# Optimization experiments

Measured on AMD Instinct MI355X. Metric: run time of the kernel, lower is better.

Reference implementation:

```python
import jax, jax.numpy as jnp
import numpy as np

B, T, D_IN, D_RNN, D_HID, D_OUT = 4096, 512, 16, 64, 128, 1

def setup_inputs() -> dict:
    key = jax.random.key(0)
    ks = jax.random.split(key, 8)
    s = 0.05  # RandomNormal init stddev
    return {
        "x":  jax.random.normal(ks[0], (B, T, D_IN), jnp.float32),
        "Wx": jax.random.normal(ks[1], (D_IN, D_RNN), jnp.float32) * s,
        "Wh": jax.random.normal(ks[2], (D_RNN, D_RNN), jnp.float32) * s,
        "b":  jnp.zeros((D_RNN,), jnp.float32),
        "W1": jax.random.normal(ks[3], (3 * D_RNN, D_HID), jnp.float32) * s,
        "b1": jnp.zeros((D_HID,), jnp.float32),
        "W2": jax.random.normal(ks[4], (D_HID, D_OUT), jnp.float32) * s,
        "b2": jnp.zeros((D_OUT,), jnp.float32),
    }

def reference(x, Wx, Wh, b, W1, b1, W2, b2):
    # SimpleRNN: h_t = tanh(x_t @ Wx + h_{t-1} @ Wh + b)
    batch = x.shape[0]
    xw = jnp.einsum('bti,ih->tbh', x, Wx) + b  # precompute input projection, time-major
    h0 = jnp.zeros((batch, Wh.shape[0]), x.dtype)

    def step(h, xw_t):
        h_new = jnp.tanh(xw_t + h @ Wh)
        return h_new, h_new

    _, hs = jax.lax.scan(step, h0, xw)          # hs: [T, B, rnn_dim]
    last3 = jnp.transpose(hs[-3:], (1, 0, 2))   # [B, 3, rnn_dim]
    out = jnp.tanh(last3.reshape(batch, -1))    # flatten + tanh
    # dropout is identity at inference
    out = jnp.tanh(out @ W1 + b1)
    out = out @ W2 + b2
    return out
```

## Files before the change

kernel.cpp:

```cpp
#include <hip/hip_runtime.h>
#include <cstdint>
#include <cstddef>

#define TSEQ 512
#define DRNN 64
#define DIN  16
#define FSTRIDE 66

typedef float    f32x4 __attribute__((ext_vector_type(4)));
typedef unsigned u32x4 __attribute__((ext_vector_type(4)));
typedef _Float16 f16x8 __attribute__((ext_vector_type(8)));

#define MFMA16(A, B, C) __builtin_amdgcn_mfma_f32_16x16x32_f16((A), (B), (C), 0, 0, 0)

__device__ __forceinline__ unsigned packh(float a, float b) {
    return __builtin_bit_cast(unsigned, __builtin_amdgcn_cvt_pkrtz(a, b));
}
__device__ __forceinline__ float tanh_fast(float x) {
    float e = __builtin_amdgcn_exp2f(x * 2.885390082f);
    float r = __builtin_amdgcn_rcpf(1.0f + e);
    return __builtin_fmaf(-2.0f, r, 1.0f);
}
__device__ __forceinline__ float tanh_pre(float d) {
    float e = __builtin_amdgcn_exp2f(d);
    float r = __builtin_amdgcn_rcpf(1.0f + e);
    return __builtin_fmaf(-2.0f, r, 1.0f);
}

#define STEPF(I, PR, PW, FS, REFILL, TB) do {                                 \
    u32x4 r0_ = *(const u32x4*)&PR[(g * 16 + li) * 4];                        \
    u32x4 r1_ = *(const u32x4*)&PR[((4 + g) * 16 + li) * 4];                  \
    f32x4 xc_ = xacc[I];                                                      \
    if (REFILL) {                                                             \
        f32x4 xv_ = xreg[I];                                                  \
        u32x4 bx_ = { packh(xv_[0], xv_[1]), packh(xv_[2], xv_[3]), 0u, 0u }; \
        xacc[I] = MFMA16(WxF, __builtin_bit_cast(f16x8, bx_), bfrS);          \
        int tl_ = (TB) + 32 + (I); if (tl_ > TSEQ - 1) tl_ = TSEQ - 1;        \
        xreg[I] = *(const f32x4*)(xrow + (size_t)tl_ * DIN);                  \
    }                                                                         \
    f16x8 Bh0_ = __builtin_bit_cast(f16x8, r0_);                              \
    f16x8 Bh1_ = __builtin_bit_cast(f16x8, r1_);                              \
    f32x4 P_ = MFMA16(WhF0, Bh0_, xc_);                                       \
    f32x4 Q_ = MFMA16(WhF1, Bh1_, zero4);                                     \
    f32x4 d_ = P_ + Q_;                                                       \
    float v0_ = tanh_pre(d_[0]), v1_ = tanh_pre(d_[1]);                       \
    float v2_ = tanh_pre(d_[2]), v3_ = tanh_pre(d_[3]);                       \
    { uint2 wv_; wv_.x = packh(v0_, v1_); wv_.y = packh(v2_, v3_);            \
      *(uint2*)&PW[((((w >> 1) * 4 + g) * 16 + li) * 4) + (w & 1) * 2] = wv_; }\
    if ((FS) >= 0) {                                                          \
        float* fp_ = &feat[((FS) * 16 + li) * FSTRIDE + 16 * w + 4 * g];      \
        fp_[0] = tanh_fast(v0_); fp_[1] = tanh_fast(v1_);                     \
        fp_[2] = tanh_fast(v2_); fp_[3] = tanh_fast(v3_);                     \
    }                                                                         \
    asm volatile("s_waitcnt lgkmcnt(0)" ::: "memory");                        \
    __builtin_amdgcn_sched_barrier(0);                                        \
    __builtin_amdgcn_s_barrier();                                             \
    __builtin_amdgcn_sched_barrier(0);                                        \
} while (0)

__global__ __launch_bounds__(256, 1) void rnn_w4(
    const float* __restrict__ X,
    const float* __restrict__ Wx,
    const float* __restrict__ Wh,
    const float* __restrict__ bias,
    const float* __restrict__ W1,
    const float* __restrict__ b1,
    const float* __restrict__ W2,
    const float* __restrict__ b2,
    float* __restrict__ out)
{
    __shared__ unsigned hxn[2][512];
    __shared__ float feat[3 * 16 * FSTRIDE];
    __shared__ float wpart[4][16];

    const int tid  = threadIdx.x;
    const int w    = tid >> 6;
    const int lane = tid & 63;
    const int li   = lane & 15;
    const int g    = lane >> 4;
    const int b0   = blockIdx.x * 16;
    const f32x4 zero4 = {0.f, 0.f, 0.f, 0.f};
    const float S = 2.885390082f;

    f16x8 WhF0, WhF1;
    {
        float wv[8];
        #pragma unroll
        for (int e = 0; e < 8; ++e) {
            int k = (e < 4 ? 4 * g + e : 16 + 4 * g + (e - 4));
            wv[e] = S * Wh[k * DRNN + 16 * w + li];
        }
        u32x4 u = { packh(wv[0],wv[1]), packh(wv[2],wv[3]),
                    packh(wv[4],wv[5]), packh(wv[6],wv[7]) };
        WhF0 = __builtin_bit_cast(f16x8, u);
        #pragma unroll
        for (int e = 0; e < 8; ++e) {
            int k = 32 + (e < 4 ? 4 * g + e : 16 + 4 * g + (e - 4));
            wv[e] = S * Wh[k * DRNN + 16 * w + li];
        }
        u32x4 v = { packh(wv[0],wv[1]), packh(wv[2],wv[3]),
                    packh(wv[4],wv[5]), packh(wv[6],wv[7]) };
        WhF1 = __builtin_bit_cast(f16x8, v);
    }
    f16x8 WxF;
    {
        float wv[4];
        #pragma unroll
        for (int e = 0; e < 4; ++e)
            wv[e] = S * Wx[(4 * g + e) * DRNN + 16 * w + li];
        u32x4 u = { packh(wv[0],wv[1]), packh(wv[2],wv[3]), 0u, 0u };
        WxF = __builtin_bit_cast(f16x8, u);
    }
    f32x4 bfrS;
    {
        f32x4 b = *(const f32x4*)(bias + 16 * w + 4 * g);
        bfrS = b * S;
    }

    const float* xrow = X + (size_t)(b0 + li) * TSEQ * DIN + 4 * g;
    f32x4 xreg[16], xacc[16];

    for (int idx = tid; idx < 2 * 512; idx += 256)
        (&hxn[0][0])[idx] = 0u;

    #pragma unroll
    for (int i = 0; i < 16; ++i)
        xreg[i] = *(const f32x4*)(xrow + (size_t)i * DIN);
    #pragma unroll
    for (int i = 0; i < 16; ++i) {
        f32x4 xv = xreg[i];
        u32x4 bx = { packh(xv[0], xv[1]), packh(xv[2], xv[3]), 0u, 0u };
        xacc[i] = MFMA16(WxF, __builtin_bit_cast(f16x8, bx), bfrS);
    }
    #pragma unroll
    for (int i = 0; i < 16; ++i)
        xreg[i] = *(const f32x4*)(xrow + (size_t)(16 + i) * DIN);
    __syncthreads();

    unsigned* hx0 = &hxn[0][0];
    unsigned* hx1 = &hxn[1][0];

    for (int tb = 0; tb < TSEQ - 16; tb += 16) {
        STEPF( 0, hx0, hx1, -1, 1, tb);
        STEPF( 1, hx1, hx0, -1, 1, tb);
        STEPF( 2, hx0, hx1, -1, 1, tb);
        STEPF( 3, hx1, hx0, -1, 1, tb);
        STEPF( 4, hx0, hx1, -1, 1, tb);
        STEPF( 5, hx1, hx0, -1, 1, tb);
        STEPF( 6, hx0, hx1, -1, 1, tb);
        STEPF( 7, hx1, hx0, -1, 1, tb);
        STEPF( 8, hx0, hx1, -1, 1, tb);
        STEPF( 9, hx1, hx0, -1, 1, tb);
        STEPF(10, hx0, hx1, -1, 1, tb);
        STEPF(11, hx1, hx0, -1, 1, tb);
        STEPF(12, hx0, hx1, -1, 1, tb);
        STEPF(13, hx1, hx0, -1, 1, tb);
        STEPF(14, hx0, hx1, -1, 1, tb);
        STEPF(15, hx1, hx0, -1, 1, tb);
    }
    STEPF( 0, hx0, hx1, -1, 0, 0);
    STEPF( 1, hx1, hx0, -1, 0, 0);
    STEPF( 2, hx0, hx1, -1, 0, 0);
    STEPF( 3, hx1, hx0, -1, 0, 0);
    STEPF( 4, hx0, hx1, -1, 0, 0);
    STEPF( 5, hx1, hx0, -1, 0, 0);
    STEPF( 6, hx0, hx1, -1, 0, 0);
    STEPF( 7, hx1, hx0, -1, 0, 0);
    STEPF( 8, hx0, hx1, -1, 0, 0);
    STEPF( 9, hx1, hx0, -1, 0, 0);
    STEPF(10, hx0, hx1, -1, 0, 0);
    STEPF(11, hx1, hx0, -1, 0, 0);
    STEPF(12, hx0, hx1, -1, 0, 0);
    STEPF(13, hx1, hx0,  0, 0, 0);
    STEPF(14, hx0, hx1,  1, 0, 0);
    STEPF(15, hx1, hx0,  2, 0, 0);

    __syncthreads();
    const int r  = tid & 15;
    const int hc = tid >> 4;
    float acc8[8];
    #pragma unroll
    for (int u = 0; u < 8; ++u) acc8[u] = b1[hc * 8 + u];
    for (int s = 0; s < 3; ++s) {
        for (int kk = 0; kk < 64; ++kk) {
            float f = feat[(s * 16 + r) * FSTRIDE + kk];
            const float* wr = &W1[(s * 64 + kk) * 128 + hc * 8];
            f32x4 w0  = *(const f32x4*)wr;
            f32x4 w1v = *(const f32x4*)(wr + 4);
            acc8[0] += f * w0[0];  acc8[1] += f * w0[1];
            acc8[2] += f * w0[2];  acc8[3] += f * w0[3];
            acc8[4] += f * w1v[0]; acc8[5] += f * w1v[1];
            acc8[6] += f * w1v[2]; acc8[7] += f * w1v[3];
        }
    }
    float p = 0.f;
    #pragma unroll
    for (int u = 0; u < 8; ++u) p += tanh_fast(acc8[u]) * W2[hc * 8 + u];
    p += __shfl_xor(p, 16);
    p += __shfl_xor(p, 32);
    if (g == 0) wpart[w][li] = p;
    __syncthreads();
    if (tid < 16)
        out[b0 + tid] = wpart[0][tid] + wpart[1][tid] + wpart[2][tid]
                      + wpart[3][tid] + b2[0];
}

extern "C" void kernel_launch(void* const* d_in, const int* in_sizes, int n_in,
                              void* d_out, int out_size, void* d_ws, size_t ws_size,
                              hipStream_t stream) {
    const float* X    = (const float*)d_in[0];
    const float* Wx   = (const float*)d_in[1];
    const float* Wh   = (const float*)d_in[2];
    const float* bias = (const float*)d_in[3];
    const float* W1   = (const float*)d_in[4];
    const float* b1   = (const float*)d_in[5];
    const float* W2   = (const float*)d_in[6];
    const float* b2   = (const float*)d_in[7];
    rnn_w4<<<256, 256, 0, stream>>>(X, Wx, Wh, bias, W1, b1, W2, b2, (float*)d_out);
}
```

Before: 112.0 us.

## Run each 16-row RNN block in one wavefront with register-resident hidden state

Each block of 16 batch rows now runs in a single 64-lane wave instead of four waves. All four output tiles of the recurrence are computed per wave, and the hidden state is fed back through registers. This relies on the MFMA output layout matching the B-operand layout, so there is no LDS exchange and no per-timestep barrier. The MLP head also moves to MFMA using the features kept in registers. The trade-off is four times more serial MFMA and tanh work per wave, with fewer waves in flight across the GPU. Each timestep's critical path becomes a chain of dependent MFMAs instead of a barrier round trip.

```diff
diff --git a/kernel.cpp b/kernel.cpp
--- a/kernel.cpp
+++ b/kernel.cpp
@@ -5,7 +5,6 @@
 #define TSEQ 512
 #define DRNN 64
 #define DIN  16
-#define FSTRIDE 66
 
 typedef float    f32x4 __attribute__((ext_vector_type(4)));
 typedef unsigned u32x4 __attribute__((ext_vector_type(4)));
@@ -15,6 +14,10 @@
 
 __device__ __forceinline__ unsigned packh(float a, float b) {
     return __builtin_bit_cast(unsigned, __builtin_amdgcn_cvt_pkrtz(a, b));
+}
+__device__ __forceinline__ f16x8 mkf(unsigned w0, unsigned w1, unsigned w2, unsigned w3) {
+    u32x4 u = {w0, w1, w2, w3};
+    return __builtin_bit_cast(f16x8, u);
 }
 __device__ __forceinline__ float tanh_fast(float x) {
     float e = __builtin_amdgcn_exp2f(x * 2.885390082f);
@@ -27,38 +30,54 @@
     return __builtin_fmaf(-2.0f, r, 1.0f);
 }
 
-#define STEPF(I, PR, PW, FS, REFILL, TB) do {                                 \
-    u32x4 r0_ = *(const u32x4*)&PR[(g * 16 + li) * 4];                        \
-    u32x4 r1_ = *(const u32x4*)&PR[((4 + g) * 16 + li) * 4];                  \
-    f32x4 xc_ = xacc[I];                                                      \
-    if (REFILL) {                                                             \
-        f32x4 xv_ = xreg[I];                                                  \
-        u32x4 bx_ = { packh(xv_[0], xv_[1]), packh(xv_[2], xv_[3]), 0u, 0u }; \
-        xacc[I] = MFMA16(WxF, __builtin_bit_cast(f16x8, bx_), bfrS);          \
-        int tl_ = (TB) + 32 + (I); if (tl_ > TSEQ - 1) tl_ = TSEQ - 1;        \
-        xreg[I] = *(const f32x4*)(xrow + (size_t)tl_ * DIN);                  \
+#define STEPA(I, FS, T, CLAMP) do {                                           \
+                      \
+    f32x4 xv_ = xreg[I];                                                      \
+    f16x8 Bx_ = mkf(packh(xv_[0], xv_[1]), packh(xv_[2], xv_[3]), 0u, 0u);    \
+    f32x4 xn0_ = MFMA16(WxF0, Bx_, bfr0);                                     \
+    f32x4 xn1_ = MFMA16(WxF1, Bx_, bfr1);                                     \
+    f32x4 xn2_ = MFMA16(WxF2, Bx_, bfr2);                                     \
+    f32x4 xn3_ = MFMA16(WxF3, Bx_, bfr3);                                     \
+    { int tl_ = (T) + 9;                                                      \
+      if (CLAMP) { if (tl_ > TSEQ - 1) tl_ = TSEQ - 1; }                      \
+      xreg[I] = *(const f32x4*)(xrow + (size_t)tl_ * DIN); }                  \
+                                          \
+    f32x4 d0_ = MFMA16(WhB0, Bh1, MFMA16(WhA0, Bh0, xc0));                    \
+    f32x4 d1_ = MFMA16(WhB1, Bh1, MFMA16(WhA1, Bh0, xc1));                    \
+    f32x4 d2_ = MFMA16(WhB2, Bh1, MFMA16(WhA2, Bh0, xc2));                    \
+    f32x4 d3_ = MFMA16(WhB3, Bh1, MFMA16(WhA3, Bh0, xc3));                    \
+    float v00_ = tanh_pre(d0_[0]), v01_ = tanh_pre(d0_[1]);                   \
+    float v02_ = tanh_pre(d0_[2]), v03_ = tanh_pre(d0_[3]);                   \
+    float v10_ = tanh_pre(d1_[0]), v11_ = tanh_pre(d1_[1]);                   \
+    float v12_ = tanh_pre(d1_[2]), v13_ = tanh_pre(d1_[3]);                   \
+    Bh0 = mkf(packh(v00_, v01_), packh(v02_, v03_),                           \
+              packh(v10_, v11_), packh(v12_, v13_));                          \
+    float v20_ = tanh_pre(d2_[0]), v21_ = tanh_pre(d2_[1]);                   \
+    float v22_ = tanh_pre(d2_[2]), v23_ = tanh_pre(d2_[3]);                   \
+    float v30_ = tanh_pre(d3_[0]), v31_ = tanh_pre(d3_[1]);                   \
+    float v32_ = tanh_pre(d3_[2]), v33_ = tanh_pre(d3_[3]);                   \
+    Bh1 = mkf(packh(v20_, v21_), packh(v22_, v23_),                           \
+              packh(v30_, v31_), packh(v32_, v33_));                          \
+    if ((FS) >= 0) {                                                          \
+        float f00_ = tanh_fast(v00_), f01_ = tanh_fast(v01_);                 \
+        float f02_ = tanh_fast(v02_), f03_ = tanh_fast(v03_);                 \
+        float f10_ = tanh_fast(v10_), f11_ = tanh_fast(v11_);                 \
+        float f12_ = tanh_fast(v12_), f13_ = tanh_fast(v13_);                 \
+        float f20_ = tanh_fast(v20_), f21_ = tanh_fast(v21_);                 \
+        float f22_ = tanh_fast(v22_), f23_ = tanh_fast(v23_);                 \
+        float f30_ = tanh_fast(v30_), f31_ = tanh_fast(v31_);                 \
+        float f32_ = tanh_fast(v32_), f33_ = tanh_fast(v33_);                 \
+        featF[(FS) >= 0 ? 2 * (FS) : 0] =                                     \
+            mkf(packh(f00_, f01_), packh(f02_, f03_),                         \
+                packh(f10_, f11_), packh(f12_, f13_));                        \
+        featF[(FS) >= 0 ? 2 * (FS) + 1 : 0] =                                 \
+            mkf(packh(f20_, f21_), packh(f22_, f23_),                         \
+                packh(f30_, f31_), packh(f32_, f33_));                        \
     }                                                                         \
-    f16x8 Bh0_ = __builtin_bit_cast(f16x8, r0_);                              \
-    f16x8 Bh1_ = __builtin_bit_cast(f16x8, r1_);                              \
-    f32x4 P_ = MFMA16(WhF0, Bh0_, xc_);                                       \
-    f32x4 Q_ = MFMA16(WhF1, Bh1_, zero4);                                     \
-    f32x4 d_ = P_ + Q_;                                                       \
-    float v0_ = tanh_pre(d_[0]), v1_ = tanh_pre(d_[1]);                       \
-    float v2_ = tanh_pre(d_[2]), v3_ = tanh_pre(d_[3]);                       \
-    { uint2 wv_; wv_.x = packh(v0_, v1_); wv_.y = packh(v2_, v3_);            \
-      *(uint2*)&PW[((((w >> 1) * 4 + g) * 16 + li) * 4) + (w & 1) * 2] = wv_; }\
-    if ((FS) >= 0) {                                                          \
-        float* fp_ = &feat[((FS) * 16 + li) * FSTRIDE + 16 * w + 4 * g];      \
-        fp_[0] = tanh_fast(v0_); fp_[1] = tanh_fast(v1_);                     \
-        fp_[2] = tanh_fast(v2_); fp_[3] = tanh_fast(v3_);                     \
-    }                                                                         \
-    asm volatile("s_waitcnt lgkmcnt(0)" ::: "memory");                        \
-    __builtin_amdgcn_sched_barrier(0);                                        \
-    __builtin_amdgcn_s_barrier();                                             \
-    __builtin_amdgcn_sched_barrier(0);                                        \
+    xc0 = xn0_; xc1 = xn1_; xc2 = xn2_; xc3 = xn3_;                           \
 } while (0)
 
-__global__ __launch_bounds__(256, 1) void rnn_w4(
+__global__ __launch_bounds__(64, 1) void rnn_nb(
     const float* __restrict__ X,
     const float* __restrict__ Wx,
     const float* __restrict__ Wh,
@@ -69,140 +88,112 @@
     const float* __restrict__ b2,
     float* __restrict__ out)
 {
-    __shared__ unsigned hxn[2][512];
-    __shared__ float feat[3 * 16 * FSTRIDE];
-    __shared__ float wpart[4][16];
-
-    const int tid  = threadIdx.x;
-    const int w    = tid >> 6;
-    const int lane = tid & 63;
+    const int lane = threadIdx.x & 63;
     const int li   = lane & 15;
     const int g    = lane >> 4;
     const int b0   = blockIdx.x * 16;
-    const f32x4 zero4 = {0.f, 0.f, 0.f, 0.f};
-    const float S = 2.885390082f;
-
-    f16x8 WhF0, WhF1;
-    {
+    const float S  = 2.885390082f;
+
+    auto loadWh = [&](int c, int mt) -> f16x8 {
         float wv[8];
         #pragma unroll
         for (int e = 0; e < 8; ++e) {
-            int k = (e < 4 ? 4 * g + e : 16 + 4 * g + (e - 4));
-            wv[e] = S * Wh[k * DRNN + 16 * w + li];
+            int k = c * 32 + (e < 4 ? 4 * g + e : 16 + 4 * g + (e - 4));
+            wv[e] = S * Wh[k * DRNN + 16 * mt + li];
         }
-        u32x4 u = { packh(wv[0],wv[1]), packh(wv[2],wv[3]),
-                    packh(wv[4],wv[5]), packh(wv[6],wv[7]) };
-        WhF0 = __builtin_bit_cast(f16x8, u);
-        #pragma unroll
-        for (int e = 0; e < 8; ++e) {
-            int k = 32 + (e < 4 ? 4 * g + e : 16 + 4 * g + (e - 4));
-            wv[e] = S * Wh[k * DRNN + 16 * w + li];
-        }
-        u32x4 v = { packh(wv[0],wv[1]), packh(wv[2],wv[3]),
-                    packh(wv[4],wv[5]), packh(wv[6],wv[7]) };
-        WhF1 = __builtin_bit_cast(f16x8, v);
-    }
-    f16x8 WxF;
-    {
+        return mkf(packh(wv[0], wv[1]), packh(wv[2], wv[3]),
+                   packh(wv[4], wv[5]), packh(wv[6], wv[7]));
+    };
+    f16x8 WhA0 = loadWh(0, 0), WhA1 = loadWh(0, 1),
+          WhA2 = loadWh(0, 2), WhA3 = loadWh(0, 3);
+    f16x8 WhB0 = loadWh(1, 0), WhB1 = loadWh(1, 1),
+          WhB2 = loadWh(1, 2), WhB3 = loadWh(1, 3);
+
+    auto loadWx = [&](int mt) -> f16x8 {
         float wv[4];
         #pragma unroll
         for (int e = 0; e < 4; ++e)
-            wv[e] = S * Wx[(4 * g + e) * DRNN + 16 * w + li];
-        u32x4 u = { packh(wv[0],wv[1]), packh(wv[2],wv[3]), 0u, 0u };
-        WxF = __builtin_bit_cast(f16x8, u);
+            wv[e] = S * Wx[(4 * g + e) * DRNN + 16 * mt + li];
+        return mkf(packh(wv[0], wv[1]), packh(wv[2], wv[3]), 0u, 0u);
+    };
+    f16x8 WxF0 = loadWx(0), WxF1 = loadWx(1), WxF2 = loadWx(2), WxF3 = loadWx(3);
+
+    f32x4 bfr0 = *(const f32x4*)(bias + 0 + 4 * g) * S;
+    f32x4 bfr1 = *(const f32x4*)(bias + 16 + 4 * g) * S;
+    f32x4 bfr2 = *(const f32x4*)(bias + 32 + 4 * g) * S;
+    f32x4 bfr3 = *(const f32x4*)(bias + 48 + 4 * g) * S;
+
+    const float* xrow = X + (size_t)(b0 + li) * TSEQ * DIN + 4 * g;
+    f32x4 xreg[8];
+    #pragma unroll
+    for (int i = 1; i < 8; ++i)
+        xreg[i] = *(const f32x4*)(xrow + (size_t)i * DIN);
+    xreg[0] = *(const f32x4*)(xrow + (size_t)8 * DIN);
+
+    f32x4 xc0, xc1, xc2, xc3;
+    {
+        f32x4 x0v = *(const f32x4*)(xrow);
+        f16x8 Bx0 = mkf(packh(x0v[0], x0v[1]), packh(x0v[2], x0v[3]), 0u, 0u);
+        xc0 = MFMA16(WxF0, Bx0, bfr0);
+        xc1 = MFMA16(WxF1, Bx0, bfr1);
+        xc2 = MFMA16(WxF2, Bx0, bfr2);
+        xc3 = MFMA16(WxF3, Bx0, bfr3);
     }
-    f32x4 bfrS;
-    {
-        f32x4 b = *(const f32x4*)(bias + 16 * w + 4 * g);
-        bfrS = b * S;
+    f16x8 Bh0 = mkf(0u, 0u, 0u, 0u), Bh1 = mkf(0u, 0u, 0u, 0u);
+    f16x8 featF[6];
+    #pragma unroll
+    for (int i = 0; i < 6; ++i) featF[i] = mkf(0u, 0u, 0u, 0u);
+
+    for (int tb = 0; tb < TSEQ - 16; tb += 8) {
+        STEPA(1, -1, tb + 0, 0);
+        STEPA(2, -1, tb + 1, 0);
+        STEPA(3, -1, tb + 2, 0);
+        STEPA(4, -1, tb + 3, 0);
+        STEPA(5, -1, tb + 4, 0);
+        STEPA(6, -1, tb + 5, 0);
+        STEPA(7, -1, tb + 6, 0);
+        STEPA(0, -1, tb + 7, 0);
     }
-
-    const float* xrow = X + (size_t)(b0 + li) * TSEQ * DIN + 4 * g;
-    f32x4 xreg[16], xacc[16];
-
-    for (int idx = tid; idx < 2 * 512; idx += 256)
-        (&hxn[0][0])[idx] = 0u;
-
-    #pragma unroll
-    for (int i = 0; i < 16; ++i)
-        xreg[i] = *(const f32x4*)(xrow + (size_t)i * DIN);
-    #pragma unroll
-    for (int i = 0; i < 16; ++i) {
-        f32x4 xv = xreg[i];
-        u32x4 bx = { packh(xv[0], xv[1]), packh(xv[2], xv[3]), 0u, 0u };
-        xacc[i] = MFMA16(WxF, __builtin_bit_cast(f16x8, bx), bfrS);
-    }
-    #pragma unroll
-    for (int i = 0; i < 16; ++i)
-        xreg[i] = *(const f32x4*)(xrow + (size_t)(16 + i) * DIN);
-    __syncthreads();
-
-    unsigned* hx0 = &hxn[0][0];
-    unsigned* hx1 = &hxn[1][0];
-
-    for (int tb = 0; tb < TSEQ - 16; tb += 16) {
-        STEPF( 0, hx0, hx1, -1, 1, tb);
-        STEPF( 1, hx1, hx0, -1, 1, tb);
-        STEPF( 2, hx0, hx1, -1, 1, tb);
-        STEPF( 3, hx1, hx0, -1, 1, tb);
-        STEPF( 4, hx0, hx1, -1, 1, tb);
-        STEPF( 5, hx1, hx0, -1, 1, tb);
-        STEPF( 6, hx0, hx1, -1, 1, tb);
-        STEPF( 7, hx1, hx0, -1, 1, tb);
-        STEPF( 8, hx0, hx1, -1, 1, tb);
-        STEPF( 9, hx1, hx0, -1, 1, tb);
-        STEPF(10, hx0, hx1, -1, 1, tb);
-        STEPF(11, hx1, hx0, -1, 1, tb);
-        STEPF(12, hx0, hx1, -1, 1, tb);
-        STEPF(13, hx1, hx0, -1, 1, tb);
-        STEPF(14, hx0, hx1, -1, 1, tb);
-        STEPF(15, hx1, hx0, -1, 1, tb);
-    }
-    STEPF( 0, hx0, hx1, -1, 0, 0);
-    STEPF( 1, hx1, hx0, -1, 0, 0);
-    STEPF( 2, hx0, hx1, -1, 0, 0);
-    STEPF( 3, hx1, hx0, -1, 0, 0);
-    STEPF( 4, hx0, hx1, -1, 0, 0);
-    STEPF( 5, hx1, hx0, -1, 0, 0);
-    STEPF( 6, hx0, hx1, -1, 0, 0);
-    STEPF( 7, hx1, hx0, -1, 0, 0);
-    STEPF( 8, hx0, hx1, -1, 0, 0);
-    STEPF( 9, hx1, hx0, -1, 0, 0);
-    STEPF(10, hx0, hx1, -1, 0, 0);
-    STEPF(11, hx1, hx0, -1, 0, 0);
-    STEPF(12, hx0, hx1, -1, 0, 0);
-    STEPF(13, hx1, hx0,  0, 0, 0);
-    STEPF(14, hx0, hx1,  1, 0, 0);
-    STEPF(15, hx1, hx0,  2, 0, 0);
-
-    __syncthreads();
-    const int r  = tid & 15;
-    const int hc = tid >> 4;
-    float acc8[8];
-    #pragma unroll
-    for (int u = 0; u < 8; ++u) acc8[u] = b1[hc * 8 + u];
-    for (int s = 0; s < 3; ++s) {
-        for (int kk = 0; kk < 64; ++kk) {
-            float f = feat[(s * 16 + r) * FSTRIDE + kk];
-            const float* wr = &W1[(s * 64 + kk) * 128 + hc * 8];
-            f32x4 w0  = *(const f32x4*)wr;
-            f32x4 w1v = *(const f32x4*)(wr + 4);
-            acc8[0] += f * w0[0];  acc8[1] += f * w0[1];
-            acc8[2] += f * w0[2];  acc8[3] += f * w0[3];
-            acc8[4] += f * w1v[0]; acc8[5] += f * w1v[1];
-            acc8[6] += f * w1v[2]; acc8[7] += f * w1v[3];
-        }
-    }
+    STEPA(1, -1, 496, 1);
+    STEPA(2, -1, 497, 1);
+    STEPA(3, -1, 498, 1);
+    STEPA(4, -1, 499, 1);
+    STEPA(5, -1, 500, 1);
+    STEPA(6, -1, 501, 1);
+    STEPA(7, -1, 502, 1);
+    STEPA(0, -1, 503, 1);
+    STEPA(1, -1, 504, 1);
+    STEPA(2, -1, 505, 1);
+    STEPA(3, -1, 506, 1);
+    STEPA(4, -1, 507, 1);
+    STEPA(5, -1, 508, 1);
+    STEPA(6,  0, 509, 1);
+    STEPA(7,  1, 510, 1);
+    STEPA(0,  2, 511, 1);
+
     float p = 0.f;
     #pragma unroll
-    for (int u = 0; u < 8; ++u) p += tanh_fast(acc8[u]) * W2[hc * 8 + u];
+    for (int nt = 0; nt < 8; ++nt) {
+        f32x4 a = *(const f32x4*)(b1 + nt * 16 + 4 * g);
+        #pragma unroll
+        for (int c6 = 0; c6 < 6; ++c6) {
+            float wv[8];
+            #pragma unroll
+            for (int e = 0; e < 8; ++e) {
+                int k = c6 * 32 + (e < 4 ? 4 * g + e : 16 + 4 * g + (e - 4));
+                wv[e] = W1[k * 128 + nt * 16 + li];
+            }
+            f16x8 wf = mkf(packh(wv[0], wv[1]), packh(wv[2], wv[3]),
+                           packh(wv[4], wv[5]), packh(wv[6], wv[7]));
+            a = MFMA16(wf, featF[c6], a);
+        }
+        f32x4 w2v = *(const f32x4*)(W2 + nt * 16 + 4 * g);
+        p += tanh_fast(a[0]) * w2v[0] + tanh_fast(a[1]) * w2v[1]
+           + tanh_fast(a[2]) * w2v[2] + tanh_fast(a[3]) * w2v[3];
+    }
     p += __shfl_xor(p, 16);
     p += __shfl_xor(p, 32);
-    if (g == 0) wpart[w][li] = p;
-    __syncthreads();
-    if (tid < 16)
-        out[b0 + tid] = wpart[0][tid] + wpart[1][tid] + wpart[2][tid]
-                      + wpart[3][tid] + b2[0];
+    if (lane < 16) out[b0 + lane] = p + b2[0];
 }
 
 extern "C" void kernel_launch(void* const* d_in, const int* in_sizes, int n_in,
@@ -216,5 +207,5 @@
     const float* b1   = (const float*)d_in[5];
     const float* W2   = (const float*)d_in[6];
     const float* b2   = (const float*)d_in[7];
-    rnn_w4<<<256, 256, 0, stream>>>(X, Wx, Wh, bias, W1, b1, W2, b2, (float*)d_out);
-}
+    rnn_nb<<<256, 64, 0, stream>>>(X, Wx, Wh, bias, W1, b1, W2, b2, (float*)d_out);
+}
```

Result: slower. 162.9 us (+45.4%).
